# Kernel tuning notes

Hardware: AMD Instinct MI355X
Metric: run time of the kernel (lower is better)

Reference implementation:

```python
import jax, jax.numpy as jnp
import numpy as np

LN_EPS = 1e-5

def _ln(x, g, b):
    m = x.mean(-1, keepdims=True)
    v = x.var(-1, keepdims=True)
    return (x - m) * jax.lax.rsqrt(v + LN_EPS) * g + b

def _sru_layer(x, W, vc, bias, g, be):
    # x: (L, B, d); W: (d, k*h) with k=3 (d==h) or k=4 (d!=h)
    L, B, _ = x.shape
    h = vc.shape[0] // 2
    xn = _ln(x, g, be)
    k = W.shape[1] // h
    U = (xn @ W).reshape(L, B, k, h)
    u0, u1, u2 = U[:, :, 0], U[:, :, 1], U[:, :, 2]
    res = U[:, :, 3] if k == 4 else xn
    vf, vr = vc[:h], vc[h:]
    bf, br = bias[:h], bias[h:]
    def step(c, inp):
        a0, a1, a2, rt = inp
        f = jax.nn.sigmoid(a1 + vf * c + bf)
        r = jax.nn.sigmoid(a2 + vr * c + br)
        c2 = f * c + (1.0 - f) * a0
        return c2, r * c2 + (1.0 - r) * rt
    _, hs = jax.lax.scan(step, jnp.zeros((B, h), x.dtype), (u0, u1, u2, res))
    return hs  # (L, B, h)

def _lstm(x, Wih, Whh, bih, bhh):
    # x: (L, B, d); PyTorch gate order i, f, g, o
    L, B, _ = x.shape
    H = Whh.shape[1]
    pre = x @ Wih.T + (bih + bhh)  # (L, B, 4H)
    def step(carry, p):
        hp, cp = carry
        gates = p + hp @ Whh.T
        i, f, g, o = jnp.split(gates, 4, axis=-1)
        c = jax.nn.sigmoid(f) * cp + jax.nn.sigmoid(i) * jnp.tanh(g)
        hn = jax.nn.sigmoid(o) * jnp.tanh(c)
        return (hn, c), hn
    z = jnp.zeros((B, H), x.dtype)
    _, hs = jax.lax.scan(step, (z, z), pre)
    return hs

def setup_inputs() -> dict:
    key = jax.random.key(0)
    ks = jax.random.split(key, 12)
    B, T, F, H, LS, V = 16, 1024, 128, 1024, 1024, 1000
    s = 0.05
    inp = {}
    inp['x'] = jax.random.normal(ks[0], (B, T, F), dtype=jnp.float32)
    # first SRU layer (input F != H -> k=4)
    inp['w0'] = jax.random.normal(ks[1], (F, 4 * H), dtype=jnp.float32) * s
    inp['vc0'] = jax.random.normal(ks[2], (2 * H,), dtype=jnp.float32) * s
    inp['b0'] = jnp.zeros((2 * H,), jnp.float32)
    inp['g0'] = jnp.ones((F,), jnp.float32)
    inp['be0'] = jnp.zeros((F,), jnp.float32)
    # 6 stacked SRU layers with d==h (3 remaining first_layer + 3 sru_layers)
    inp['Ws'] = jax.random.normal(ks[3], (6, H, 3 * H), dtype=jnp.float32) * s
    inp['VCs'] = jax.random.normal(ks[4], (6, 2 * H), dtype=jnp.float32) * s
    inp['Bs'] = jnp.zeros((6, 2 * H), jnp.float32)
    inp['Gs'] = jnp.ones((6, H), jnp.float32)
    inp['Bes'] = jnp.zeros((6, H), jnp.float32)
    # LSTM
    inp['Wih'] = jax.random.normal(ks[5], (4 * LS, H), dtype=jnp.float32) * s
    inp['Whh'] = jax.random.normal(ks[6], (4 * LS, LS), dtype=jnp.float32) * s
    inp['bih'] = jnp.zeros((4 * LS,), jnp.float32)
    inp['bhh'] = jnp.zeros((4 * LS,), jnp.float32)
    # classifier: LayerNorm + Linear(no bias) to V+1
    inp['gh'] = jnp.ones((LS,), jnp.float32)
    inp['bh'] = jnp.zeros((LS,), jnp.float32)
    inp['Wout'] = jax.random.normal(ks[7], (LS, V + 1), dtype=jnp.float32) * s
    return inp

def reference(x, w0, vc0, b0, g0, be0, Ws, VCs, Bs, Gs, Bes,
              Wih, Whh, bih, bhh, gh, bh, Wout):
    t = jnp.transpose(x, (1, 0, 2))  # (T, B, F)
    t = _sru_layer(t, w0, vc0, b0, g0, be0)
    for i in range(3):
        t = _sru_layer(t, Ws[i], VCs[i], Bs[i], Gs[i], Bes[i])
    # AvgPool1d(kernel=2, stride=2) over time
    L = t.shape[0]
    t = t[: (L // 2) * 2].reshape(L // 2, 2, t.shape[1], t.shape[2]).mean(axis=1)
    for i in range(3, 6):
        t = _sru_layer(t, Ws[i], VCs[i], Bs[i], Gs[i], Bes[i])
    t = _lstm(t, Wih, Whh, bih, bhh)
    t = jnp.transpose(t, (1, 0, 2))  # (B, T/2, lstm_dim)
    return _ln(t, gh, bh) @ Wout  # (B, T/2, n_vocab+1)
```

## Files before the change

kernel.cpp:

```cpp
#include <hip/hip_runtime.h>

typedef __bf16 bf16x8 __attribute__((ext_vector_type(8)));
typedef float f32x4 __attribute__((ext_vector_type(4)));

__device__ __forceinline__ unsigned short f2bf(float f) {
  unsigned u = __builtin_bit_cast(unsigned, f);
  u += 0x7fffu + ((u >> 16) & 1u);
  return (unsigned short)(u >> 16);
}
__device__ __forceinline__ float bf2f(unsigned short h) {
  unsigned u = ((unsigned)h) << 16;
  return __builtin_bit_cast(float, u);
}
__device__ __forceinline__ float sigmoidf_(float x) {
  return 1.f / (1.f + __expf(-x));
}
__device__ __forceinline__ float tanhf_(float x) {
  return 1.f - 2.f / (__expf(2.f * x) + 1.f);
}
__device__ __forceinline__ void gload16(const unsigned short* g, unsigned short* l) {
  __builtin_amdgcn_global_load_lds((const __attribute__((address_space(1))) void*)g,
                                   (__attribute__((address_space(3))) void*)l, 16, 0, 0);
}


__global__ __launch_bounds__(256) void k_castf(const float* __restrict__ src,
                                               unsigned short* __restrict__ dst, int n4) {
  int i = blockIdx.x * 256 + threadIdx.x;
  if (i < n4) {
    float4 v = ((const float4*)src)[i];
    ushort4 o;
    o.x = f2bf(v.x); o.y = f2bf(v.y); o.z = f2bf(v.z); o.w = f2bf(v.w);
    ((ushort4*)dst)[i] = o;
  }
}

__global__ void k_cast_t(const float* __restrict__ src, unsigned short* __restrict__ dst,
                         int K, int N) {
  __shared__ float tile[32][33];
  int nx = blockIdx.x * 32, ky = blockIdx.y * 32;
  int tx = threadIdx.x, ty = threadIdx.y;
  #pragma unroll
  for (int j = 0; j < 32; j += 8) {
    int n = nx + tx, k = ky + ty + j;
    tile[ty + j][tx] = (n < N) ? src[(long)k * N + n] : 0.f;
  }
  __syncthreads();
  #pragma unroll
  for (int j = 0; j < 32; j += 8) {
    int n = nx + ty + j, k = ky + tx;
    dst[(long)n * K + k] = f2bf(tile[tx][ty + j]);
  }
}


__global__ __launch_bounds__(128) void k_ln0(const float* __restrict__ x,
                                             unsigned short* __restrict__ out,
                                             const float* __restrict__ g,
                                             const float* __restrict__ be) {
  int row = blockIdx.x;
  int t = row >> 4, b = row & 15;
  const float* src = x + ((long)b * 1024 + t) * 128;
  int i = threadIdx.x;
  float v = src[i];
  float s = v, q = v * v;
  #pragma unroll
  for (int off = 32; off > 0; off >>= 1) {
    s += __shfl_down(s, off);
    q += __shfl_down(q, off);
  }
  __shared__ float red[4];
  int wv = i >> 6;
  if ((i & 63) == 0) { red[wv] = s; red[2 + wv] = q; }
  __syncthreads();
  float S = red[0] + red[1], Q = red[2] + red[3];
  float mean = S * (1.f / 128.f);
  float var = Q * (1.f / 128.f) - mean * mean;
  float rs = rsqrtf(var + 1e-5f);
  out[(long)row * 128 + i] = f2bf((v - mean) * rs * g[i] + be[i]);
}

__global__ __launch_bounds__(256) void k_ln(const float* __restrict__ in,
                                            unsigned short* __restrict__ out16,
                                            const float* __restrict__ g,
                                            const float* __restrict__ be, int avg) {
  int row = blockIdx.x;
  int tid = threadIdx.x;
  int col = tid * 4;
  float xv[4];
  if (avg) {
    int l = row >> 4, b = row & 15;
    const float* r0 = in + ((long)(2 * l) * 16 + b) * 1024;
    const float* r1 = r0 + 16 * 1024;
    float4 a = *(const float4*)(r0 + col);
    float4 bb = *(const float4*)(r1 + col);
    xv[0] = 0.5f * (a.x + bb.x);
    xv[1] = 0.5f * (a.y + bb.y);
    xv[2] = 0.5f * (a.z + bb.z);
    xv[3] = 0.5f * (a.w + bb.w);
  } else {
    float4 a = *(const float4*)(in + (long)row * 1024 + col);
    xv[0] = a.x; xv[1] = a.y; xv[2] = a.z; xv[3] = a.w;
  }
  float s = xv[0] + xv[1] + xv[2] + xv[3];
  float q = xv[0]*xv[0] + xv[1]*xv[1] + xv[2]*xv[2] + xv[3]*xv[3];
  #pragma unroll
  for (int off = 32; off > 0; off >>= 1) {
    s += __shfl_down(s, off);
    q += __shfl_down(q, off);
  }
  __shared__ float red[8];
  int wv = tid >> 6;
  if ((tid & 63) == 0) { red[wv] = s; red[4 + wv] = q; }
  __syncthreads();
  float S = red[0] + red[1] + red[2] + red[3];
  float Q = red[4] + red[5] + red[6] + red[7];
  float mean = S * (1.f / 1024.f);
  float var = Q * (1.f / 1024.f) - mean * mean;
  float rs = rsqrtf(var + 1e-5f);
  ushort4 o;
  o.x = f2bf((xv[0] - mean) * rs * g[col + 0] + be[col + 0]);
  o.y = f2bf((xv[1] - mean) * rs * g[col + 1] + be[col + 1]);
  o.z = f2bf((xv[2] - mean) * rs * g[col + 2] + be[col + 2]);
  o.w = f2bf((xv[3] - mean) * rs * g[col + 3] + be[col + 3]);
  *(ushort4*)(out16 + (long)row * 1024 + col) = o;
}

template <int MODE>
__global__ __launch_bounds__(256) void k_gemm(const unsigned short* __restrict__ A,
                                              const unsigned short* __restrict__ Bt,
                                              void* __restrict__ Cout,
                                              const float* __restrict__ bias1,
                                              const float* __restrict__ bias2,
                                              int M, int N, int K) {
  __shared__ unsigned short As[128][64];
  __shared__ unsigned short Bs[128][64];
  const int bn = blockIdx.x * 128, bm = blockIdx.y * 128;
  const int tid = threadIdx.x;
  const int wave = tid >> 6, lane = tid & 63;
  const int wm = (wave >> 1) * 64, wn = (wave & 1) * 64;
  const int l15 = lane & 15, kq = lane >> 4;
  f32x4 acc[4][4] = {};
  const int r0 = tid >> 3;
  const int c0 = (tid & 7) * 8;
  const unsigned short* Ap = A + (long)(bm + r0) * K + c0;
  const unsigned short* Bp = Bt + (long)(bn + r0) * K + c0;
  for (int kb = 0; kb < K; kb += 64) {
    #pragma unroll
    for (int i = 0; i < 4; i++) {
      gload16(Ap + (long)(i * 32) * K + kb, &As[i * 32 + r0][c0]);
      gload16(Bp + (long)(i * 32) * K + kb, &Bs[i * 32 + r0][c0]);
    }
    __syncthreads();
    #pragma unroll
    for (int kk = 0; kk < 2; kk++) {
      const int kcol = kk * 32 + kq * 8;
      bf16x8 a[4], b[4];
      #pragma unroll
      for (int m = 0; m < 4; m++) a[m] = *(const bf16x8*)&As[wm + m * 16 + l15][kcol];
      #pragma unroll
      for (int n = 0; n < 4; n++) b[n] = *(const bf16x8*)&Bs[wn + n * 16 + l15][kcol];
      #pragma unroll
      for (int m = 0; m < 4; m++)
        #pragma unroll
        for (int n = 0; n < 4; n++)
          acc[m][n] = __builtin_amdgcn_mfma_f32_16x16x32_bf16(a[m], b[n], acc[m][n], 0, 0, 0);
    }
    __syncthreads();
  }
  #pragma unroll
  for (int m = 0; m < 4; m++)
    #pragma unroll
    for (int n = 0; n < 4; n++) {
      #pragma unroll
      for (int r = 0; r < 4; r++) {
        int gm = bm + wm + m * 16 + kq * 4 + r;
        int gn = bn + wn + n * 16 + l15;
        float v = acc[m][n][r];
        if (MODE == 0) {
          ((float*)Cout)[(long)gm * N + gn] = v;
        } else if (MODE == 1) {
          v += bias1[gn] + bias2[gn];
          ((float*)Cout)[(long)gm * N + gn] = v;
        } else {
          if (gn < 1001) {
            long oi = ((long)(gm & 15) * 512 + (gm >> 4)) * 1001 + gn;
            ((float*)Cout)[oi] = v;
          }
        }
      }
    }
}

__global__ __launch_bounds__(64) void k_scan(const float* __restrict__ U,
                                             const unsigned short* __restrict__ Res16,
                                             const float* __restrict__ vc,
                                             const float* __restrict__ bias,
                                             float* __restrict__ Hout,
                                             unsigned short* __restrict__ H16,
                                             float* __restrict__ cbuf,
                                             int Lc, int k4, int first) {
  int tid = blockIdx.x * 64 + threadIdx.x;
  int b = tid >> 10, hc = tid & 1023;
  float vf = vc[hc], vr = vc[1024 + hc];
  float bfv = bias[hc], brv = bias[1024 + hc];
  const int k = k4 ? 4 : 3;
  const long strideT = 16L * k * 1024;
  const long base0 = (long)b * k * 1024 + hc;
  const long rbase = (long)b * 1024 + hc;
  const long rstride = 16 * 1024;
  float c = first ? 0.f : cbuf[tid];
  for (int t0 = 0; t0 < Lc; t0 += 16) {
    float u0[16], u1[16], u2[16], rr[16];
    #pragma unroll
    for (int j = 0; j < 16; j++) {
      long o = base0 + (long)(t0 + j) * strideT;
      u0[j] = U[o];
      u1[j] = U[o + 1024];
      u2[j] = U[o + 2048];
      rr[j] = k4 ? U[o + 3072] : bf2f(Res16[rbase + (long)(t0 + j) * rstride]);
    }
    #pragma unroll
    for (int j = 0; j < 16; j++) {
      float f = sigmoidf_(u1[j] + vf * c + bfv);
      float r = sigmoidf_(u2[j] + vr * c + brv);
      c = f * c + (1.f - f) * u0[j];
      float h = r * c + (1.f - r) * rr[j];
      long oo = rbase + (long)(t0 + j) * rstride;
      if (Hout) Hout[oo] = h;
      if (H16) H16[oo] = f2bf(h);
    }
  }
  cbuf[tid] = c;
}

__global__ __launch_bounds__(256) void k_lstm_step(
    const unsigned short* __restrict__ Whhb,
    const float* __restrict__ Prep,
    const unsigned short* __restrict__ hin,
    unsigned short* __restrict__ hout,
    float* __restrict__ cst,
    float* __restrict__ HsOutp) {
  const int tid = threadIdx.x;
  const int wave = tid >> 6, lane = tid & 63;
  const int j = blockIdx.x;
  const int c0 = j * 4;
  const int l15 = lane & 15, kq = lane >> 4;
  const int wrow = (l15 >> 2) * 1024 + c0 + (l15 & 3);
  f32x4 acc = {0.f, 0.f, 0.f, 0.f};
  const unsigned short* hp = hin + l15 * 1024 + wave * 256 + kq * 8;
  const unsigned short* wp = Whhb + (long)wrow * 1024 + wave * 256 + kq * 8;
  #pragma unroll
  for (int kb = 0; kb < 256; kb += 32) {
    bf16x8 a = *(const bf16x8*)(hp + kb);
    bf16x8 w = *(const bf16x8*)(wp + kb);
    acc = __builtin_amdgcn_mfma_f32_16x16x32_bf16(a, w, acc, 0, 0, 0);
  }
  __shared__ float P[4][16][16];
  __shared__ float G[16][16];
  #pragma unroll
  for (int r = 0; r < 4; r++) {
    int m = kq * 4 + r;
    P[wave][m][l15] = acc[r];
  }
  __syncthreads();
  {
    int m = tid >> 4, col = tid & 15;
    int gate = col >> 2, ch = c0 + (col & 3);
    float pre = Prep[(long)m * 4096 + gate * 1024 + ch];
    G[m][col] = P[0][m][col] + P[1][m][col] + P[2][m][col] + P[3][m][col] + pre;
  }
  __syncthreads();
  if (tid < 64) {
    int m = tid & 15, chl = tid >> 4;
    float ig = G[m][0 * 4 + chl];
    float fg = G[m][1 * 4 + chl];
    float gg = G[m][2 * 4 + chl];
    float og = G[m][3 * 4 + chl];
    long ci = (long)m * 1024 + c0 + chl;
    float cold = cst[ci];
    float cn = sigmoidf_(fg) * cold + sigmoidf_(ig) * tanhf_(gg);
    float hn = sigmoidf_(og) * tanhf_(cn);
    cst[ci] = cn;
    hout[ci] = f2bf(hn);
    HsOutp[(long)m * 1024 + c0 + chl] = hn;
  }
}


extern "C" void kernel_launch(void* const* d_in, const int* in_sizes, int n_in,
                              void* d_out, int out_size, void* d_ws, size_t ws_size,
                              hipStream_t stream) {
  const float* x    = (const float*)d_in[0];
  const float* w0   = (const float*)d_in[1];
  const float* vc0  = (const float*)d_in[2];
  const float* b0   = (const float*)d_in[3];
  const float* g0   = (const float*)d_in[4];
  const float* be0  = (const float*)d_in[5];
  const float* Ws   = (const float*)d_in[6];
  const float* VCs  = (const float*)d_in[7];
  const float* Bsi  = (const float*)d_in[8];
  const float* Gs   = (const float*)d_in[9];
  const float* Bes  = (const float*)d_in[10];
  const float* Wih  = (const float*)d_in[11];
  const float* Whh  = (const float*)d_in[12];
  const float* bih  = (const float*)d_in[13];
  const float* bhh  = (const float*)d_in[14];
  const float* gh   = (const float*)d_in[15];
  const float* bh   = (const float*)d_in[16];
  const float* Wout = (const float*)d_in[17];

  char* ws = (char*)d_ws;
  size_t off = 0;
  auto alloc = [&](size_t bytes) {
    size_t r = off;
    off += (bytes + 255) & ~(size_t)255;
    return r;
  };
  unsigned short* W0t   = (unsigned short*)(ws + alloc(4096UL * 128 * 2));
  unsigned short* Wst   = (unsigned short*)(ws + alloc(6UL * 3072 * 1024 * 2));
  unsigned short* Wihb  = (unsigned short*)(ws + alloc(4096UL * 1024 * 2));
  unsigned short* Whhb  = (unsigned short*)(ws + alloc(4096UL * 1024 * 2));
  unsigned short* Woutt = (unsigned short*)(ws + alloc(1024UL * 1024 * 2));
  unsigned short* Xn    = (unsigned short*)(ws + alloc(16384UL * 1024 * 2));
  float*          Hbuf  = (float*)(ws + alloc(16384UL * 1024 * 4));
  float*          Ubuf  = (float*)(ws + alloc(4096UL * 4096 * 4));
  unsigned short* hb0   = (unsigned short*)(ws + alloc(16UL * 1024 * 2));
  unsigned short* hb1   = (unsigned short*)(ws + alloc(16UL * 1024 * 2));
  float*          cst   = (float*)(ws + alloc(16UL * 1024 * 4));
  float*          cscan = (float*)(ws + alloc(16UL * 1024 * 4));
  float*          HsOut = Hbuf;
  unsigned short* H16l6 = Xn + 8192L * 1024;
  unsigned short* LNout = Xn;

  k_cast_t<<<dim3(4096 / 32, 128 / 32), dim3(32, 8), 0, stream>>>(w0, W0t, 128, 4096);
  for (int i = 0; i < 6; i++)
    k_cast_t<<<dim3(3072 / 32, 1024 / 32), dim3(32, 8), 0, stream>>>(
        Ws + (long)i * 1024 * 3072, Wst + (long)i * 3072 * 1024, 1024, 3072);
  k_cast_t<<<dim3(1024 / 32, 1024 / 32), dim3(32, 8), 0, stream>>>(Wout, Woutt, 1024, 1001);
  k_castf<<<4096, 256, 0, stream>>>(Wih, Wihb, 4096 * 1024 / 4);
  k_castf<<<4096, 256, 0, stream>>>(Whh, Whhb, 4096 * 1024 / 4);
  hipMemsetAsync(hb0, 0, 32768 + 32768 + 65536, stream);

  const int CH_T = 256;
  const int CH_R = CH_T * 16;

  k_ln0<<<16384, 128, 0, stream>>>(x, Xn, g0, be0);
  for (int c = 0; c < 4; c++) {
    k_gemm<0><<<dim3(4096 / 128, CH_R / 128), 256, 0, stream>>>(
        Xn + (long)c * CH_R * 128, W0t, Ubuf, nullptr, nullptr, CH_R, 4096, 128);
    k_scan<<<256, 64, 0, stream>>>(Ubuf, nullptr, vc0, b0,
                                   Hbuf + (long)c * CH_R * 1024, nullptr, cscan,
                                   CH_T, 1, c == 0);
  }

  for (int i = 0; i < 6; i++) {
    int L = (i < 3) ? 1024 : 512;
    int rows = L * 16;
    int avg = (i == 3) ? 1 : 0;
    k_ln<<<rows, 256, 0, stream>>>(Hbuf, Xn, Gs + i * 1024, Bes + i * 1024, avg);
    int nch = rows / CH_R;
    for (int c = 0; c < nch; c++) {
      k_gemm<0><<<dim3(3072 / 128, CH_R / 128), 256, 0, stream>>>(
          Xn + (long)c * CH_R * 1024, Wst + (long)i * 3072 * 1024, Ubuf, nullptr, nullptr,
          CH_R, 3072, 1024);
      k_scan<<<256, 64, 0, stream>>>(Ubuf, Xn + (long)c * CH_R * 1024,
                                     VCs + i * 2048, Bsi + i * 2048,
                                     (i == 5) ? nullptr : (Hbuf + (long)c * CH_R * 1024),
                                     (i == 5) ? (H16l6 + (long)c * CH_R * 1024) : nullptr,
                                     cscan, CH_T, 0, c == 0);
    }
  }

  const int LCH_T = 256, LCH_R = LCH_T * 16;
  for (int c = 0; c < 2; c++) {
    k_gemm<1><<<dim3(4096 / 128, LCH_R / 128), 256, 0, stream>>>(
        H16l6 + (long)c * LCH_R * 1024, Wihb, Ubuf, bih, bhh, LCH_R, 4096, 1024);
    for (int tl = 0; tl < LCH_T; tl++) {
      int tg = c * LCH_T + tl;
      unsigned short* hin = (tg & 1) ? hb1 : hb0;
      unsigned short* hout = (tg & 1) ? hb0 : hb1;
      k_lstm_step<<<256, 256, 0, stream>>>(Whhb, Ubuf + (long)tl * 16 * 4096, hin, hout,
                                           cst, HsOut + (long)tg * 16 * 1024);
    }
  }

  k_ln<<<8192, 256, 0, stream>>>(HsOut, LNout, gh, bh, 0);
  k_gemm<2><<<dim3(1024 / 128, 8192 / 128), 256, 0, stream>>>(LNout, Woutt, d_out, nullptr,
                                                              nullptr, 8192, 1024, 1024);
}
```

Measured before the change: 6.234 ms.

## Single-wave LSTM step with shuffle gate exchange; double-buffer SRU scan loads

The LSTM step kernel drops from four waves splitting K with an LDS reduction and two barriers to one wave doing the full K=1024 MFMA chain. Gates are gathered with lane shuffles, and the preactivation and cell-state loads are issued before the matmul. The SRU scan kernel now double-buffers its per-timestep U loads, fetching the next 16 steps while computing the current 16. In exchange the step kernel loses K-parallelism: each wave runs a dependent chain of 32 MFMAs, and the scan uses more registers.

```diff
diff --git a/kernel.cpp b/kernel.cpp
--- a/kernel.cpp
+++ b/kernel.cpp
@@ -204,86 +204,90 @@
   int b = tid >> 10, hc = tid & 1023;
   float vf = vc[hc], vr = vc[1024 + hc];
   float bfv = bias[hc], brv = bias[1024 + hc];
-  const int k = k4 ? 4 : 3;
-  const long strideT = 16L * k * 1024;
-  const long base0 = (long)b * k * 1024 + hc;
+  const long strideT = 16L * (k4 ? 4 : 3) * 1024;
+  const long base0 = (long)b * (k4 ? 4 : 3) * 1024 + hc;
   const long rbase = (long)b * 1024 + hc;
   const long rstride = 16 * 1024;
   float c = first ? 0.f : cbuf[tid];
-  for (int t0 = 0; t0 < Lc; t0 += 16) {
-    float u0[16], u1[16], u2[16], rr[16];
-    #pragma unroll
-    for (int j = 0; j < 16; j++) {
-      long o = base0 + (long)(t0 + j) * strideT;
-      u0[j] = U[o];
-      u1[j] = U[o + 1024];
-      u2[j] = U[o + 2048];
-      rr[j] = k4 ? U[o + 3072] : bf2f(Res16[rbase + (long)(t0 + j) * rstride]);
-    }
-    #pragma unroll
-    for (int j = 0; j < 16; j++) {
-      float f = sigmoidf_(u1[j] + vf * c + bfv);
-      float r = sigmoidf_(u2[j] + vr * c + brv);
-      c = f * c + (1.f - f) * u0[j];
-      float h = r * c + (1.f - r) * rr[j];
-      long oo = rbase + (long)(t0 + j) * rstride;
-      if (Hout) Hout[oo] = h;
-      if (H16) H16[oo] = f2bf(h);
-    }
-  }
+  float u0a[16], u1a[16], u2a[16], rra[16];
+  float u0b[16], u1b[16], u2b[16], rrb[16];
+
+#define LOADX(A0, A1, A2, RR, T0)                                              \
+  _Pragma("unroll") for (int j = 0; j < 16; j++) {                             \
+    long o = base0 + (long)((T0) + j) * strideT;                               \
+    A0[j] = U[o];                                                              \
+    A1[j] = U[o + 1024];                                                       \
+    A2[j] = U[o + 2048];                                                       \
+    RR[j] = k4 ? U[o + 3072] : bf2f(Res16[rbase + (long)((T0) + j) * rstride]);\
+  }
+#define COMPX(A0, A1, A2, RR, T0)                                              \
+  _Pragma("unroll") for (int j = 0; j < 16; j++) {                             \
+    float f = sigmoidf_(A1[j] + vf * c + bfv);                                 \
+    float r = sigmoidf_(A2[j] + vr * c + brv);                                 \
+    c = f * c + (1.f - f) * A0[j];                                             \
+    float h = r * c + (1.f - r) * RR[j];                                       \
+    long oo = rbase + (long)((T0) + j) * rstride;                              \
+    if (Hout) Hout[oo] = h;                                                    \
+    if (H16) H16[oo] = f2bf(h);                                                \
+  }
+
+  LOADX(u0a, u1a, u2a, rra, 0)
+  for (int t0 = 0; t0 < Lc; t0 += 32) {
+    if (t0 + 16 < Lc) LOADX(u0b, u1b, u2b, rrb, t0 + 16)
+    COMPX(u0a, u1a, u2a, rra, t0)
+    if (t0 + 32 < Lc) LOADX(u0a, u1a, u2a, rra, t0 + 32)
+    COMPX(u0b, u1b, u2b, rrb, t0 + 16)
+  }
+#undef LOADX
+#undef COMPX
   cbuf[tid] = c;
 }
 
-__global__ __launch_bounds__(256) void k_lstm_step(
+__global__ __launch_bounds__(64) void k_lstm_step(
     const unsigned short* __restrict__ Whhb,
     const float* __restrict__ Prep,
     const unsigned short* __restrict__ hin,
     unsigned short* __restrict__ hout,
     float* __restrict__ cst,
     float* __restrict__ HsOutp) {
-  const int tid = threadIdx.x;
-  const int wave = tid >> 6, lane = tid & 63;
+  const int lane = threadIdx.x;
   const int j = blockIdx.x;
   const int c0 = j * 4;
   const int l15 = lane & 15, kq = lane >> 4;
-  const int wrow = (l15 >> 2) * 1024 + c0 + (l15 & 3);
+  const int gate = l15 >> 2, chl = l15 & 3;
+  const int wrow = gate * 1024 + c0 + chl;
+  float pre[4], cold[4];
+  #pragma unroll
+  for (int r = 0; r < 4; r++) {
+    pre[r] = Prep[(long)(kq * 4 + r) * 4096 + wrow];
+    cold[r] = cst[(long)(kq * 4 + r) * 1024 + c0 + chl];
+  }
   f32x4 acc = {0.f, 0.f, 0.f, 0.f};
-  const unsigned short* hp = hin + l15 * 1024 + wave * 256 + kq * 8;
-  const unsigned short* wp = Whhb + (long)wrow * 1024 + wave * 256 + kq * 8;
-  #pragma unroll
-  for (int kb = 0; kb < 256; kb += 32) {
+  const unsigned short* hp = hin + l15 * 1024 + kq * 8;
+  const unsigned short* wp = Whhb + (long)wrow * 1024 + kq * 8;
+  #pragma unroll
+  for (int kb = 0; kb < 1024; kb += 32) {
     bf16x8 a = *(const bf16x8*)(hp + kb);
     bf16x8 w = *(const bf16x8*)(wp + kb);
     acc = __builtin_amdgcn_mfma_f32_16x16x32_bf16(a, w, acc, 0, 0, 0);
   }
-  __shared__ float P[4][16][16];
-  __shared__ float G[16][16];
   #pragma unroll
   for (int r = 0; r < 4; r++) {
-    int m = kq * 4 + r;
-    P[wave][m][l15] = acc[r];
-  }
-  __syncthreads();
-  {
-    int m = tid >> 4, col = tid & 15;
-    int gate = col >> 2, ch = c0 + (col & 3);
-    float pre = Prep[(long)m * 4096 + gate * 1024 + ch];
-    G[m][col] = P[0][m][col] + P[1][m][col] + P[2][m][col] + P[3][m][col] + pre;
-  }
-  __syncthreads();
-  if (tid < 64) {
-    int m = tid & 15, chl = tid >> 4;
-    float ig = G[m][0 * 4 + chl];
-    float fg = G[m][1 * 4 + chl];
-    float gg = G[m][2 * 4 + chl];
-    float og = G[m][3 * 4 + chl];
-    long ci = (long)m * 1024 + c0 + chl;
-    float cold = cst[ci];
-    float cn = sigmoidf_(fg) * cold + sigmoidf_(ig) * tanhf_(gg);
-    float hn = sigmoidf_(og) * tanhf_(cn);
-    cst[ci] = cn;
-    hout[ci] = f2bf(hn);
-    HsOutp[(long)m * 1024 + c0 + chl] = hn;
+    float v = acc[r] + pre[r];
+    int base = (lane & 48) | chl;
+    float ig = __shfl(v, base);
+    float fg = __shfl(v, base + 4);
+    float gg = __shfl(v, base + 8);
+    float og = __shfl(v, base + 12);
+    if (gate == 0) {
+      int m = kq * 4 + r;
+      float cn = sigmoidf_(fg) * cold[r] + sigmoidf_(ig) * tanhf_(gg);
+      float hn = sigmoidf_(og) * tanhf_(cn);
+      long ci = (long)m * 1024 + c0 + chl;
+      cst[ci] = cn;
+      hout[ci] = f2bf(hn);
+      HsOutp[ci] = hn;
+    }
   }
 }
 
@@ -380,8 +384,8 @@
       int tg = c * LCH_T + tl;
       unsigned short* hin = (tg & 1) ? hb1 : hb0;
       unsigned short* hout = (tg & 1) ? hb0 : hb1;
-      k_lstm_step<<<256, 256, 0, stream>>>(Whhb, Ubuf + (long)tl * 16 * 4096, hin, hout,
-                                           cst, HsOut + (long)tg * 16 * 1024);
+      k_lstm_step<<<256, 64, 0, stream>>>(Whhb, Ubuf + (long)tl * 16 * 4096, hin, hout,
+                                          cst, HsOut + (long)tg * 16 * 1024);
     }
   }
 
```

After: 7.222 ms. 1.16x slower.
